# Optimization experiments

Measured on AMD Instinct MI355X. Metric: run time of the kernel, lower is better.

## Reference

```python
import jax, jax.numpy as jnp
import numpy as np

H = 8
HID = 512
DH = HID // H
EPS = 1e-5


def _ln(x, g, b):
    mu = jnp.mean(x, axis=-1, keepdims=True)
    var = jnp.mean(jnp.square(x - mu), axis=-1, keepdims=True)
    return (x - mu) * jax.lax.rsqrt(var + EPS) * g + b


def setup_inputs() -> dict:
    key = jax.random.key(0)
    ks = jax.random.split(key, 40)
    L, M, P, D = 4096, 1024, 4096, 512

    def xav(k, shp):
        lim = np.sqrt(6.0 / (shp[0] + shp[1]))
        return jax.random.uniform(k, shp, jnp.float32, -lim, lim)

    inp = {
        'lncRNA_embedding': jax.random.normal(ks[0], (L, D), jnp.float32),
        'miRNA_embedding': jax.random.normal(ks[1], (M, D), jnp.float32),
        'protein_embedding': jax.random.normal(ks[2], (P, D), jnp.float32),
        'lncRNA_miRNA_matrix': jax.random.randint(ks[3], (L, M), 0, 2, jnp.int32),
        'protein_miRNA_matrix': jax.random.randint(ks[4], (P, M), 0, 2, jnp.int32),
    }
    names = ['Wl', 'Wm', 'Wp', 'Wql', 'Wkl', 'Wvl', 'Wqp', 'Wkp', 'Wvp']
    for i, n in enumerate(names):
        inp[n] = xav(ks[5 + i], (HID, HID))
        inp['b' + n[1:]] = jnp.zeros((HID,), jnp.float32)
    inp['Wml'] = xav(ks[20], (2 * HID, D // 2))
    inp['bml'] = jnp.zeros((D // 2,), jnp.float32)
    inp['Wmp'] = xav(ks[21], (2 * HID, D // 2))
    inp['bmp'] = jnp.zeros((D // 2,), jnp.float32)
    inp['g1'] = jnp.ones((D // 2,), jnp.float32)
    inp['be1'] = jnp.zeros((D // 2,), jnp.float32)
    inp['g2'] = jnp.ones((D // 2,), jnp.float32)
    inp['be2'] = jnp.zeros((D // 2,), jnp.float32)
    # first three linears take dim-D input (D == HID here)
    return inp


def reference(lncRNA_embedding, miRNA_embedding, protein_embedding,
              lncRNA_miRNA_matrix, protein_miRNA_matrix,
              Wl, bl, Wm, bm, Wp, bp,
              Wql, bql, Wkl, bkl, Wvl, bvl,
              Wqp, bqp, Wkp, bkp, Wvp, bvp,
              Wml, bml, Wmp, bmp, g1, be1, g2, be2):
    L = lncRNA_embedding.shape[0]
    M = miRNA_embedding.shape[0]
    P = protein_embedding.shape[0]

    lt = lncRNA_embedding @ Wl + bl          # [L, HID]
    mt = miRNA_embedding @ Wm + bm           # [M, HID]
    pt = protein_embedding @ Wp + bp         # [P, HID]

    def heads(x, W, b, n):
        return (x @ W + b).reshape(n, H, DH)

    Ql = heads(lt, Wql, bql, L)              # [L, H, DH]
    Kl = heads(mt, Wkl, bkl, M)
    Vl = heads(mt, Wvl, bvl, M)
    Qp = heads(pt, Wqp, bqp, P)
    Kp = heads(mt, Wkp, bkp, M)
    Vp = heads(mt, Wvp, bvp, M)

    scale = 1.0 / np.sqrt(DH)
    sl = jnp.einsum('lhd,mhd->hlm', Ql, Kl) * scale      # [H, L, M]
    sl = jnp.where(lncRNA_miRNA_matrix[None] == 0, -1e9, sl)
    awl = jax.nn.softmax(sl, axis=-1)

    sp = jnp.einsum('phd,mhd->hpm', Qp, Kp) * scale      # [H, P, M]
    sp = jnp.where(protein_miRNA_matrix[None] == 0, -1e9, sp)
    awp = jax.nn.softmax(sp, axis=-1)

    ctx_l = jax.nn.relu(jnp.einsum('hlm,mhd->lhd', awl, Vl).reshape(L, HID))
    ctx_p = jax.nn.relu(jnp.einsum('hpm,mhd->phd', awp, Vp).reshape(P, HID))

    mutual = jnp.einsum('hlm,hpm->lp', awl, awp) / H     # [L, P]

    fin_l = ctx_l + mutual @ ctx_p
    fin_p = ctx_p + mutual.T @ ctx_l

    out_l = _ln(jnp.concatenate([lt, fin_l], axis=-1) @ Wml + bml, g1, be1)
    out_p = _ln(jnp.concatenate([fin_p, pt], axis=-1) @ Wmp + bmp, g2, be2)
    return out_l, out_p
```

## Files before the change

### kernel.cpp

```cpp
#include <hip/hip_runtime.h>
#include <hip/hip_bf16.h>

using bf16 = __hip_bfloat16;
typedef __attribute__((ext_vector_type(8))) short short8;
typedef __attribute__((ext_vector_type(4))) float floatx4;
typedef __attribute__((ext_vector_type(8))) unsigned short ushort8;
typedef __attribute__((ext_vector_type(4))) int i32x4;
typedef __attribute__((ext_vector_type(8))) int i32x8;

__device__ __forceinline__ float b2f(unsigned short u) {
    union { unsigned int i; float f; } x; x.i = ((unsigned int)u) << 16; return x.f;
}

__device__ __forceinline__ void async16(const void* g, void* l) {
    __builtin_amdgcn_global_load_lds((const __attribute__((address_space(1))) void*)g,
                                     (__attribute__((address_space(3))) void*)l,
                                     16, 0, 0);
}

__device__ __forceinline__ unsigned char f2e4m3(float f) {
    unsigned s = (__float_as_uint(f) >> 24) & 0x80u;
    f = fminf(fabsf(f), 448.f);
    if (f < 0.015625f) {
        int d = (int)rintf(f * 512.f);
        return (unsigned char)(s | (unsigned)d);
    }
    int E = (int)((__float_as_uint(f) >> 23) & 255u) - 127;
    float ulp_inv = __uint_as_float((unsigned)(127 + 3 - E) << 23);
    int m = (int)rintf(f * ulp_inv);
    int n = (m == 16) ? ((E + 8) << 3) : (((E + 7) << 3) + (m - 8));
    if (n > 0x7E) n = 0x7E;
    return (unsigned char)(s | (unsigned)n);
}

__device__ __forceinline__ bool sniff_wave(const unsigned short* p) {
    const int lane = threadIdx.x & 63;
    int wild = 0;
#pragma unroll
    for (int j = 0; j < 4; ++j) {
        float a = fabsf(b2f(p[lane * 4 + j]));
        wild += !(a <= 1e4f);
    }
#pragma unroll
    for (int o = 1; o < 64; o <<= 1) wild += __shfl_xor(wild, o);
    return wild > 16;
}

struct Cvt { const void* src; bf16* dst; int n; };
struct PrepArgs {
    Cvt cv[18];
    const void* tsrc[11];
    bf16* tdst[11];
    const unsigned short* sn;
};

__global__ __launch_bounds__(256) void prep(PrepArgs a) {
    const bool f32 = sniff_wave(a.sn);
    const int y = blockIdx.y;
    __shared__ bf16 tile[32][33];

    if (y < 18) {
        const Cvt c = a.cv[y];
        const int stride = gridDim.x * 256 * 8;
        for (int i = (blockIdx.x * 256 + threadIdx.x) * 8; i < c.n; i += stride) {
            if (f32) {
                const float* s = (const float*)c.src + i;
#pragma unroll
                for (int j = 0; j < 8; ++j) c.dst[i + j] = __float2bfloat16(s[j]);
            } else {
                *(ushort8*)((unsigned short*)c.dst + i) =
                    *(const ushort8*)((const unsigned short*)c.src + i);
            }
        }
        return;
    }

    const int tx = threadIdx.x & 31;
    const int ty = threadIdx.x >> 5;
    if (y < 27) {
        const void* in = a.tsrc[y - 18];
        bf16* out = a.tdst[y - 18];
        const int bc = (blockIdx.x & 15) * 32;
        const int br = (blockIdx.x >> 4) * 32;
#pragma unroll
        for (int i = 0; i < 32; i += 8) {
            const size_t idx = (size_t)(br + ty + i) * 512 + bc + tx;
            tile[ty + i][tx] = f32 ? __float2bfloat16(((const float*)in)[idx])
                                   : ((const bf16*)in)[idx];
        }
        __syncthreads();
#pragma unroll
        for (int i = 0; i < 32; i += 8)
            out[(size_t)(bc + ty + i) * 512 + br + tx] = tile[tx][ty + i];
    } else {
        const void* in = a.tsrc[y - 27 + 9];
        bf16* out = a.tdst[y - 27 + 9];
        const int bc = (blockIdx.x & 7) * 32;
        const int br = (blockIdx.x >> 3) * 32;
#pragma unroll
        for (int i = 0; i < 32; i += 8) {
            const size_t idx = (size_t)(br + ty + i) * 256 + bc + tx;
            tile[ty + i][tx] = f32 ? __float2bfloat16(((const float*)in)[idx])
                                   : ((const bf16*)in)[idx];
        }
        __syncthreads();
#pragma unroll
        for (int i = 0; i < 32; i += 8)
            out[(size_t)(bc + ty + i) * 1024 + br + tx] = tile[tx][ty + i];
    }
}

struct SegTab { const bf16* W[3]; const bf16* bias[3]; bf16* C[3]; int ldc[3]; int rs[3]; };

__global__ __launch_bounds__(256) void gemm_bt_seg(
    const bf16* __restrict__ A, SegTab T, int K)
{
    constexpr int TM = 2, TN = 2;
    __align__(16) __shared__ bf16 As[64 * 64];
    __align__(16) __shared__ bf16 Bs[64 * 64];

    const int lane = threadIdx.x & 63;
    const int wv   = threadIdx.x >> 6;
    const int gm   = blockIdx.y * 64;
    const int seg  = (gm >= 5120) ? 2 : ((gm >= 4096) ? 1 : 0);
    const bf16* B  = T.W[seg];
    const bf16* bias = T.bias[seg];
    bf16* C        = T.C[seg];
    const int ldc  = T.ldc[seg];
    const int m_base = gm - T.rs[seg];
    const int n_base = blockIdx.x * 64;
    const int wm0 = (wv >> 1) * 32;
    const int wn0 = (wv & 1) * 32;

    floatx4 zero = {0.f, 0.f, 0.f, 0.f};
    floatx4 acc[TM][TN];
#pragma unroll
    for (int mt = 0; mt < TM; ++mt)
#pragma unroll
        for (int nt = 0; nt < TN; ++nt) acc[mt][nt] = zero;

    const int sr  = lane >> 3;
    const int sce = ((lane & 7) ^ sr) * 8;
    const int fr  = lane & 15;
    const int q   = lane >> 4;
    const int sw  = fr & 7;

    for (int k0 = 0; k0 < K; k0 += 64) {
#pragma unroll
        for (int cc = 0; cc < 2; ++cc) {
            const int r0t = (wv + cc * 4) * 8;
            async16(A + (size_t)(gm + r0t + sr) * 512 + k0 + sce, &As[r0t * 64]);
            async16(B + (size_t)(n_base + r0t + sr) * 512 + k0 + sce, &Bs[r0t * 64]);
        }
        __syncthreads();
#pragma unroll
        for (int s = 0; s < 2; ++s) {
            const int off = ((s * 4 + q) ^ sw) * 8;
            short8 af[TM], bfr[TN];
#pragma unroll
            for (int mt = 0; mt < TM; ++mt)
                af[mt] = *(const short8*)&As[(wm0 + mt * 16 + fr) * 64 + off];
#pragma unroll
            for (int nt = 0; nt < TN; ++nt)
                bfr[nt] = *(const short8*)&Bs[(wn0 + nt * 16 + fr) * 64 + off];
#pragma unroll
            for (int mt = 0; mt < TM; ++mt)
#pragma unroll
                for (int nt = 0; nt < TN; ++nt)
                    acc[mt][nt] = __builtin_amdgcn_mfma_f32_16x16x32_bf16(
                        af[mt], bfr[nt], acc[mt][nt], 0, 0, 0);
        }
        __syncthreads();
    }

    const int er = lane >> 4;
    const int ec = lane & 15;
#pragma unroll
    for (int nt = 0; nt < TN; ++nt) {
        const int col = n_base + wn0 + nt * 16 + ec;
        const float bv = __bfloat162float(bias[col]);
#pragma unroll
        for (int mt = 0; mt < TM; ++mt)
#pragma unroll
            for (int r = 0; r < 4; ++r) {
                const int row = m_base + wm0 + mt * 16 + er * 4 + r;
                C[(size_t)row * ldc + col] = __float2bfloat16(acc[mt][nt][r] + bv);
            }
    }
}

struct BtArgs { const bf16* A; const bf16* B; void* C; const bf16* bias;
                int lda, ldb, ldc; };
struct BtSet { BtArgs s[3]; };

template <bool F32OUT, bool REMAP2>
__global__ __launch_bounds__(256) void gemm_btx(BtSet P, int K, float scale)
{
    constexpr int TM = 2, TN = 2;
    __align__(16) __shared__ bf16 As[64 * 64];
    __align__(16) __shared__ bf16 Bs[64 * 64];

    const BtArgs g = P.s[blockIdx.z];
    int bx = blockIdx.x, by = blockIdx.y;
    if (REMAP2 && blockIdx.z == 2) {
        const int flat = by * gridDim.x + bx;
        bx = flat & 31; by = flat >> 5;
    }
    const int lane = threadIdx.x & 63;
    const int wv   = threadIdx.x >> 6;
    const int m_base = by * 64;
    const int n_base = bx * 64;
    const int wm0 = (wv >> 1) * 32;
    const int wn0 = (wv & 1) * 32;

    floatx4 zero = {0.f, 0.f, 0.f, 0.f};
    floatx4 acc[TM][TN];
#pragma unroll
    for (int mt = 0; mt < TM; ++mt)
#pragma unroll
        for (int nt = 0; nt < TN; ++nt) acc[mt][nt] = zero;

    const int sr  = lane >> 3;
    const int sce = ((lane & 7) ^ sr) * 8;
    const int fr  = lane & 15;
    const int q   = lane >> 4;
    const int sw  = fr & 7;

    for (int k0 = 0; k0 < K; k0 += 64) {
#pragma unroll
        for (int cc = 0; cc < 2; ++cc) {
            const int r0t = (wv + cc * 4) * 8;
            async16(g.A + (size_t)(m_base + r0t + sr) * g.lda + k0 + sce, &As[r0t * 64]);
            async16(g.B + (size_t)(n_base + r0t + sr) * g.ldb + k0 + sce, &Bs[r0t * 64]);
        }
        __syncthreads();
#pragma unroll
        for (int s = 0; s < 2; ++s) {
            const int off = ((s * 4 + q) ^ sw) * 8;
            short8 af[TM], bfr[TN];
#pragma unroll
            for (int mt = 0; mt < TM; ++mt)
                af[mt] = *(const short8*)&As[(wm0 + mt * 16 + fr) * 64 + off];
#pragma unroll
            for (int nt = 0; nt < TN; ++nt)
                bfr[nt] = *(const short8*)&Bs[(wn0 + nt * 16 + fr) * 64 + off];
#pragma unroll
            for (int mt = 0; mt < TM; ++mt)
#pragma unroll
                for (int nt = 0; nt < TN; ++nt)
                    acc[mt][nt] = __builtin_amdgcn_mfma_f32_16x16x32_bf16(
                        af[mt], bfr[nt], acc[mt][nt], 0, 0, 0);
        }
        __syncthreads();
    }

    const int er = lane >> 4;
    const int ec = lane & 15;
#pragma unroll
    for (int nt = 0; nt < TN; ++nt) {
        const int col = n_base + wn0 + nt * 16 + ec;
        const float bv = __bfloat162float(g.bias[col]);
#pragma unroll
        for (int mt = 0; mt < TM; ++mt)
#pragma unroll
            for (int r = 0; r < 4; ++r) {
                const int row = m_base + wm0 + mt * 16 + er * 4 + r;
                const float v = acc[mt][nt][r] * scale + bv;
                if constexpr (F32OUT)
                    ((float*)g.C)[(size_t)row * g.ldc + col] = v;
                else
                    ((bf16*)g.C)[(size_t)row * g.ldc + col] = __float2bfloat16(v);
            }
    }
}

struct ScArgs { const bf16* Q; const bf16* K; const int* mask; unsigned char* aw; };
struct ScSet { ScArgs s[2]; const bf16* vsrc[2]; unsigned char* vdst[2]; };

__global__ __launch_bounds__(256) void scores_v8(ScSet P, int ldk, float scale)
{
    __shared__ float wred[16][4];
    __shared__ float wsum[16][4];
    __shared__ float tile[32][33];

    if (blockIdx.z == 2) {
        const int flat = blockIdx.y * 256 + blockIdx.x;
        if (flat >= 1024) return;
        const int side = flat >> 9;
        const int rem  = flat & 511;
        const bf16* in = P.vsrc[side];
        unsigned char* out = P.vdst[side];
        const int bc = (rem & 15) * 32;
        const int br = (rem >> 4) * 32;
        const int tx = threadIdx.x & 31;
        const int ty = threadIdx.x >> 5;
#pragma unroll
        for (int i = 0; i < 32; i += 8)
            tile[ty + i][tx] =
                __bfloat162float(in[(size_t)(br + ty + i) * 2048 + bc + tx]) * 4.0f;
        __syncthreads();
#pragma unroll
        for (int i = 0; i < 32; i += 8)
            out[(size_t)(bc + ty + i) * 1024 + br + tx] = f2e4m3(tile[tx][ty + i]);
        return;
    }

    const ScArgs g = P.s[blockIdx.z];
    const int t    = threadIdx.x;
    const int lane = t & 63;
    const int w    = t >> 6;
    const int h    = blockIdx.y;
    const int r0   = blockIdx.x * 16;
    const int fr   = lane & 15;
    const int fq   = lane >> 4;
    const int cbase = w * 256;

    const short* Qs = (const short*)g.Q + (size_t)(r0 + fr) * 512 + h * 64 + fq * 8;
    short8 a0 = *(const short8*)(Qs);
    short8 a1 = *(const short8*)(Qs + 32);

    floatx4 accs[16];
    const short* Kb = (const short*)g.K + h * 64 + fq * 8;
#pragma unroll
    for (int c = 0; c < 16; ++c) {
        const int krow = cbase + c * 16 + fr;
        short8 b0 = *(const short8*)(Kb + (size_t)krow * ldk);
        short8 b1 = *(const short8*)(Kb + (size_t)krow * ldk + 32);
        floatx4 acc = {0.f, 0.f, 0.f, 0.f};
        acc = __builtin_amdgcn_mfma_f32_16x16x32_bf16(a0, b0, acc, 0, 0, 0);
        acc = __builtin_amdgcn_mfma_f32_16x16x32_bf16(a1, b1, acc, 0, 0, 0);
        accs[c] = acc;
    }

    float mxr[4] = {-3e38f, -3e38f, -3e38f, -3e38f};
#pragma unroll
    for (int c = 0; c < 16; ++c) {
        const int col = cbase + c * 16 + fr;
#pragma unroll
        for (int r = 0; r < 4; ++r) {
            const int row = r0 + fq * 4 + r;
            float v = (g.mask[(size_t)row * 1024 + col] == 0) ? -1e9f
                                                              : accs[c][r] * scale;
            accs[c][r] = v;
            mxr[r] = fmaxf(mxr[r], v);
        }
    }
#pragma unroll
    for (int o = 1; o < 16; o <<= 1)
#pragma unroll
        for (int r = 0; r < 4; ++r) mxr[r] = fmaxf(mxr[r], __shfl_xor(mxr[r], o));
    if (fr == 0)
#pragma unroll
        for (int r = 0; r < 4; ++r) wred[fq * 4 + r][w] = mxr[r];
    __syncthreads();

    float mx[4], sm[4] = {0.f, 0.f, 0.f, 0.f};
#pragma unroll
    for (int r = 0; r < 4; ++r) {
        const int row = fq * 4 + r;
        mx[r] = fmaxf(fmaxf(wred[row][0], wred[row][1]),
                      fmaxf(wred[row][2], wred[row][3]));
    }
#pragma unroll
    for (int c = 0; c < 16; ++c)
#pragma unroll
        for (int r = 0; r < 4; ++r) {
            float e = __expf(accs[c][r] - mx[r]);
            accs[c][r] = e;
            sm[r] += e;
        }
#pragma unroll
    for (int o = 1; o < 16; o <<= 1)
#pragma unroll
        for (int r = 0; r < 4; ++r) sm[r] += __shfl_xor(sm[r], o);
    if (fr == 0)
#pragma unroll
        for (int r = 0; r < 4; ++r) wsum[fq * 4 + r][w] = sm[r];
    __syncthreads();

    float inv[4];
#pragma unroll
    for (int r = 0; r < 4; ++r) {
        const int row = fq * 4 + r;
        inv[r] = 32.0f / (wsum[row][0] + wsum[row][1] + wsum[row][2] + wsum[row][3]);
    }
#pragma unroll
    for (int c = 0; c < 16; ++c) {
        const int col = cbase + c * 16 + fr;
#pragma unroll
        for (int r = 0; r < 4; ++r) {
            const int row = r0 + fq * 4 + r;
            g.aw[(size_t)row * 8192 + h * 1024 + col] = f2e4m3(accs[c][r] * inv[r]);
        }
    }
}

struct B8Args { const unsigned char* A; const unsigned char* B; bf16* C;
                unsigned char* CT; };
struct B8Pair { B8Args s[2]; };

__global__ __launch_bounds__(256) void gemm_bt8_ctx(
    B8Pair P, int lda, long long a_kshift, int ldb, int ldc, int ldct,
    int K, float scale)
{
    constexpr int TM = 2, TN = 2;
    __align__(16) __shared__ unsigned char As[64 * 64];
    __align__(16) __shared__ unsigned char Bs[64 * 64];

    const B8Args g = P.s[blockIdx.z];
    const int lane = threadIdx.x & 63;
    const int wv   = threadIdx.x >> 6;
    const int m_base = blockIdx.y * 64;
    const int n_base = blockIdx.x * 64;
    const unsigned char* A = g.A + (long long)blockIdx.x * a_kshift;

    const int wm0 = (wv >> 1) * 32;
    const int wn0 = (wv & 1) * 32;

    floatx4 zero = {0.f, 0.f, 0.f, 0.f};
    floatx4 acc[TM][TN];
#pragma unroll
    for (int mt = 0; mt < TM; ++mt)
#pragma unroll
        for (int nt = 0; nt < TN; ++nt) acc[mt][nt] = zero;

    const int ar = lane >> 2;
    const int ac = (((lane & 3) ^ (ar & 3)) * 16);
    const int fr = lane & 15;
    const int q  = lane >> 4;
    const int sw = fr & 3;

    for (int k0 = 0; k0 < K; k0 += 64) {
        async16(A + (size_t)(m_base + wv * 16 + ar) * lda + k0 + ac, &As[wv * 16 * 64]);
        async16(g.B + (size_t)(n_base + wv * 16 + ar) * ldb + k0 + ac, &Bs[wv * 16 * 64]);
        __syncthreads();
#pragma unroll
        for (int s = 0; s < 2; ++s) {
            const int boff = (((s * 2 + (q >> 1)) ^ sw) * 16) + (q & 1) * 8;
            long af[TM], bfr[TN];
#pragma unroll
            for (int mt = 0; mt < TM; ++mt)
                af[mt] = *(const long*)&As[(wm0 + mt * 16 + fr) * 64 + boff];
#pragma unroll
            for (int nt = 0; nt < TN; ++nt)
                bfr[nt] = *(const long*)&Bs[(wn0 + nt * 16 + fr) * 64 + boff];
#pragma unroll
            for (int mt = 0; mt < TM; ++mt)
#pragma unroll
                for (int nt = 0; nt < TN; ++nt)
                    acc[mt][nt] = __builtin_amdgcn_mfma_f32_16x16x32_fp8_fp8(
                        af[mt], bfr[nt], acc[mt][nt], 0, 0, 0);
        }
        __syncthreads();
    }

    const int er = lane >> 4;
    const int ec = lane & 15;
#pragma unroll
    for (int nt = 0; nt < TN; ++nt) {
        const int col = n_base + wn0 + nt * 16 + ec;
#pragma unroll
        for (int mt = 0; mt < TM; ++mt) {
            const int rowb = m_base + wm0 + mt * 16 + er * 4;
            unsigned int pk = 0;
#pragma unroll
            for (int r = 0; r < 4; ++r) {
                float v = fmaxf(acc[mt][nt][r] * scale, 0.f);
                g.C[(size_t)(rowb + r) * ldc + col] = __float2bfloat16(v);
                pk |= (unsigned)f2e4m3(v * 16.0f) << (8 * r);
            }
            *(unsigned int*)(g.CT + (size_t)col * ldct + rowb) = pk;
        }
    }
}

__global__ __launch_bounds__(512, 2) void gemm_mutual(
    const unsigned char* __restrict__ A, const unsigned char* __restrict__ B,
    unsigned char* __restrict__ C, unsigned char* __restrict__ CT,
    int K, float scale)
{
    constexpr int BM = 256, BN = 256;
    constexpr int TM = 8, TN = 4;

    __align__(16) __shared__ unsigned char As[2][BM * 128];
    __align__(16) __shared__ unsigned char Bs[2][BN * 128];

    const int lane = threadIdx.x & 63;
    const int wv   = threadIdx.x >> 6;
    const int m_base = blockIdx.y * BM;
    const int n_base = blockIdx.x * BN;
    const int wm0 = (wv >> 2) * 128;
    const int wn0 = (wv & 3) * 64;

    floatx4 zero = {0.f, 0.f, 0.f, 0.f};
    floatx4 acc[TM][TN];
#pragma unroll
    for (int mt = 0; mt < TM; ++mt)
#pragma unroll
        for (int nt = 0; nt < TN; ++nt) acc[mt][nt] = zero;

    const int sr = lane >> 3;
    const int sc = ((lane & 7) ^ sr) * 16;
    const int fr = lane & 15;
    const int q  = lane >> 4;
    const int sw = fr & 7;

    const int NT = K >> 7;

    auto stage = [&](int t, int b) {
        const int k0 = t << 7;
#pragma unroll
        for (int cc = 0; cc < 4; ++cc) {
            const int r0t = (wv + cc * 8) * 8;
            async16(A + (size_t)(m_base + r0t + sr) * (size_t)K + k0 + sc,
                    &As[b][r0t * 128]);
            async16(B + (size_t)(n_base + r0t + sr) * (size_t)K + k0 + sc,
                    &Bs[b][r0t * 128]);
        }
    };

    stage(0, 0);
    stage(1, 1);

    for (int t = 0; t < NT; ++t) {
        const int cur = t & 1;
        if (t + 1 < NT)
            asm volatile("s_waitcnt vmcnt(8)\n\ts_barrier" ::: "memory");
        else
            asm volatile("s_waitcnt vmcnt(0)\n\ts_barrier" ::: "memory");

        i32x8 bfr[TN];
#pragma unroll
        for (int nt = 0; nt < TN; ++nt) {
            const unsigned char* rp = &Bs[cur][(wn0 + nt * 16 + fr) * 128];
            i32x4 lo = *(const i32x4*)(rp + (((q * 2 + 0) ^ sw) * 16));
            i32x4 hi = *(const i32x4*)(rp + (((q * 2 + 1) ^ sw) * 16));
            bfr[nt] = __builtin_shufflevector(lo, hi, 0, 1, 2, 3, 4, 5, 6, 7);
        }
        __builtin_amdgcn_s_setprio(1);
#pragma unroll
        for (int mt = 0; mt < TM; ++mt) {
            const unsigned char* rp = &As[cur][(wm0 + mt * 16 + fr) * 128];
            i32x4 lo = *(const i32x4*)(rp + (((q * 2 + 0) ^ sw) * 16));
            i32x4 hi = *(const i32x4*)(rp + (((q * 2 + 1) ^ sw) * 16));
            i32x8 af = __builtin_shufflevector(lo, hi, 0, 1, 2, 3, 4, 5, 6, 7);
#pragma unroll
            for (int nt = 0; nt < TN; ++nt)
                acc[mt][nt] = __builtin_amdgcn_mfma_scale_f32_16x16x128_f8f6f4(
                    af, bfr[nt], acc[mt][nt], 0, 0, 0, 127, 0, 127);
        }
        __builtin_amdgcn_s_setprio(0);
        asm volatile("s_barrier" ::: "memory");
        if (t + 2 < NT) stage(t + 2, cur);
    }

    const int er = lane >> 4;
    const int ec = lane & 15;
#pragma unroll
    for (int nt = 0; nt < TN; ++nt) {
        const int col = n_base + wn0 + nt * 16 + ec;
#pragma unroll
        for (int mt = 0; mt < TM; ++mt) {
            const int rowb = m_base + wm0 + mt * 16 + er * 4;
            unsigned int pk = 0;
#pragma unroll
            for (int r = 0; r < 4; ++r) {
                const unsigned char qv = f2e4m3(acc[mt][nt][r] * scale);
                C[(size_t)(rowb + r) * 4096 + col] = qv;
                pk |= (unsigned)qv << (8 * r);
            }
            *(unsigned int*)(CT + (size_t)col * 4096 + rowb) = pk;
        }
    }
}

struct MxArgs { const unsigned char* A; const unsigned char* B; void* C;
                const bf16* Cz; unsigned char* CT; };
struct MxPair { MxArgs s[2]; };

template <int BM, int BN, bool ADDC0, bool FP8OUT, bool TOUT>
__global__ __launch_bounds__(256, 2) void gemm_bt8mx(
    MxPair P, int lda, int ldb, int ldc, int ldc0, int ldct, int K, float scale)
{
    constexpr int WM = BM / 2;
    constexpr int WN = BN / 2;
    constexpr int TM = WM / 16;
    constexpr int TN = WN / 16;

    __align__(16) __shared__ unsigned char As[BM * 128];
    __align__(16) __shared__ unsigned char Bs[BN * 128];

    const MxArgs g = P.s[blockIdx.z];
    const int lane = threadIdx.x & 63;
    const int wv   = threadIdx.x >> 6;
    const int m_base = blockIdx.y * BM;
    const int n_base = blockIdx.x * BN;

    const int wm0 = (wv >> 1) * WM;
    const int wn0 = (wv & 1) * WN;

    floatx4 zero = {0.f, 0.f, 0.f, 0.f};
    floatx4 acc[TM][TN];
#pragma unroll
    for (int mt = 0; mt < TM; ++mt)
#pragma unroll
        for (int nt = 0; nt < TN; ++nt) acc[mt][nt] = zero;

    const int sr = lane >> 3;
    const int sc = ((lane & 7) ^ sr) * 16;
    const int fr = lane & 15;
    const int q  = lane >> 4;
    const int sw = fr & 7;

    for (int k0 = 0; k0 < K; k0 += 128) {
#pragma unroll
        for (int cc = 0; cc < BM / 32; ++cc) {
            const int r0t = (wv + cc * 4) * 8;
            async16(g.A + (size_t)(m_base + r0t + sr) * lda + k0 + sc, &As[r0t * 128]);
        }
#pragma unroll
        for (int cc = 0; cc < BN / 32; ++cc) {
            const int r0t = (wv + cc * 4) * 8;
            async16(g.B + (size_t)(n_base + r0t + sr) * ldb + k0 + sc, &Bs[r0t * 128]);
        }
        __syncthreads();

        i32x8 af[TM];
#pragma unroll
        for (int mt = 0; mt < TM; ++mt) {
            const unsigned char* rp = &As[(wm0 + mt * 16 + fr) * 128];
            i32x4 lo = *(const i32x4*)(rp + (((q * 2 + 0) ^ sw) * 16));
            i32x4 hi = *(const i32x4*)(rp + (((q * 2 + 1) ^ sw) * 16));
            af[mt] = __builtin_shufflevector(lo, hi, 0, 1, 2, 3, 4, 5, 6, 7);
        }
#pragma unroll
        for (int nt = 0; nt < TN; ++nt) {
            const unsigned char* rp = &Bs[(wn0 + nt * 16 + fr) * 128];
            i32x4 lo = *(const i32x4*)(rp + (((q * 2 + 0) ^ sw) * 16));
            i32x4 hi = *(const i32x4*)(rp + (((q * 2 + 1) ^ sw) * 16));
            i32x8 bf8 = __builtin_shufflevector(lo, hi, 0, 1, 2, 3, 4, 5, 6, 7);
#pragma unroll
            for (int mt = 0; mt < TM; ++mt)
                acc[mt][nt] = __builtin_amdgcn_mfma_scale_f32_16x16x128_f8f6f4(
                    af[mt], bf8, acc[mt][nt], 0, 0, 0, 127, 0, 127);
        }
        __syncthreads();
    }

    const int er = lane >> 4;
    const int ec = lane & 15;
#pragma unroll
    for (int nt = 0; nt < TN; ++nt) {
        const int col = n_base + wn0 + nt * 16 + ec;
#pragma unroll
        for (int mt = 0; mt < TM; ++mt) {
            const int rowb = m_base + wm0 + mt * 16 + er * 4;
            unsigned int pk = 0;
#pragma unroll
            for (int r = 0; r < 4; ++r) {
                float v = acc[mt][nt][r] * scale;
                if constexpr (ADDC0)
                    v += __bfloat162float(g.Cz[(size_t)(rowb + r) * ldc0 + col]);
                if constexpr (FP8OUT) {
                    const unsigned char qv = f2e4m3(v);
                    ((unsigned char*)g.C)[(size_t)(rowb + r) * ldc + col] = qv;
                    if constexpr (TOUT) pk |= (unsigned)qv << (8 * r);
                } else {
                    ((bf16*)g.C)[(size_t)(rowb + r) * ldc + col] = __float2bfloat16(v);
                }
            }
            if constexpr (TOUT)
                *(unsigned int*)(g.CT + (size_t)col * ldct + rowb) = pk;
        }
    }
}

__global__ __launch_bounds__(256) void ln_all(
    const float* __restrict__ X,
    const bf16* __restrict__ g1, const bf16* __restrict__ be1,
    const bf16* __restrict__ g2, const bf16* __restrict__ be2,
    void* __restrict__ out, const unsigned short* __restrict__ sn)
{
    const bool f32 = sniff_wave(sn);
    const int lane = threadIdx.x & 63;
    const int wv   = threadIdx.x >> 6;
    const int row  = blockIdx.x * 4 + wv;
    const bf16* gg = (row >= 4096) ? g2 : g1;
    const bf16* bb = (row >= 4096) ? be2 : be1;
    const float* x = X + (size_t)row * 256;
    float v[4], s = 0.f, s2 = 0.f;
#pragma unroll
    for (int i = 0; i < 4; ++i) {
        v[i] = x[lane + 64 * i];
        s += v[i]; s2 += v[i] * v[i];
    }
#pragma unroll
    for (int o = 1; o < 64; o <<= 1) { s += __shfl_xor(s, o); s2 += __shfl_xor(s2, o); }
    const float mu  = s * (1.0f / 256.0f);
    const float var = fmaxf(s2 * (1.0f / 256.0f) - mu * mu, 0.0f);
    const float inv = rsqrtf(var + 1e-5f);
#pragma unroll
    for (int i = 0; i < 4; ++i) {
        const int c = lane + 64 * i;
        const float y = (v[i] - mu) * inv * __bfloat162float(gg[c]) + __bfloat162float(bb[c]);
        if (f32) ((float*)out)[(size_t)row * 256 + c] = y;
        else     ((bf16*)out)[(size_t)row * 256 + c] = __float2bfloat16(y);
    }
}

extern "C" void kernel_launch(void* const* d_in, const int* in_sizes, int n_in,
                              void* d_out, int out_size, void* d_ws, size_t ws_size,
                              hipStream_t stream)
{
    const int L = 4096, Mm = 1024, P = 4096;

    const int* mask_l = (const int*)d_in[3];
    const int* mask_p = (const int*)d_in[4];
    const unsigned short* sn = (const unsigned short*)d_in[0];

    char* ws = (char*)d_ws;
    size_t off = 0;
    auto alloc = [&](size_t bytes) {
        void* p = ws + off; off += (bytes + 255) & ~(size_t)255; return p;
    };

    bf16* wt_all = (bf16*)alloc((size_t)9 * 512 * 512 * 2);
    bf16* WmlT   = (bf16*)alloc(1024 * 256 * 2);
    bf16* WmpT   = (bf16*)alloc(1024 * 256 * 2);
    bf16* b_l    = (bf16*)alloc(512 * 2);
    bf16* b_m    = (bf16*)alloc(512 * 2);
    bf16* b_p    = (bf16*)alloc(512 * 2);
    bf16* b_ql   = (bf16*)alloc(512 * 2);
    bf16* b_qp   = (bf16*)alloc(512 * 2);
    bf16* bcat   = (bf16*)alloc(2048 * 2);
    bf16* bml_c  = (bf16*)alloc(256 * 2);
    bf16* bmp_c  = (bf16*)alloc(256 * 2);
    bf16* g1c    = (bf16*)alloc(256 * 2);
    bf16* be1c   = (bf16*)alloc(256 * 2);
    bf16* g2c    = (bf16*)alloc(256 * 2);
    bf16* be2c   = (bf16*)alloc(256 * 2);
    bf16* emb_all = (bf16*)alloc((size_t)(L + Mm + P) * 512 * 2);
    bf16* embl   = emb_all;
    bf16* embm   = emb_all + (size_t)L * 512;
    bf16* embp   = embm + (size_t)Mm * 512;
    bf16* cat_l  = (bf16*)alloc((size_t)L * 1024 * 2);
    bf16* cat_p  = (bf16*)alloc((size_t)P * 1024 * 2);
    bf16* mt     = (bf16*)alloc((size_t)Mm * 512 * 2);
    bf16* Ql     = (bf16*)alloc((size_t)L * 512 * 2);
    bf16* Qp     = (bf16*)alloc((size_t)P * 512 * 2);
    bf16* kvcat  = (bf16*)alloc((size_t)Mm * 2048 * 2);
    unsigned char* V8lT = (unsigned char*)alloc((size_t)512 * Mm);
    unsigned char* V8pT = (unsigned char*)alloc((size_t)512 * Mm);
    bf16* ctx_l  = (bf16*)alloc((size_t)L * 512 * 2);
    bf16* ctx_p  = (bf16*)alloc((size_t)P * 512 * 2);
    unsigned char* ctx8lT = (unsigned char*)alloc((size_t)512 * L);
    unsigned char* ctx8pT = (unsigned char*)alloc((size_t)512 * P);
    unsigned char* mutual8  = (unsigned char*)alloc((size_t)L * P);
    unsigned char* mutual8T = (unsigned char*)alloc((size_t)L * P);
    unsigned char* awl8 = (unsigned char*)alloc((size_t)L * 8192);
    unsigned char* awp8 = (unsigned char*)alloc((size_t)P * 8192);
    float* tmp1 = (float*)awp8;

    PrepArgs pa;
    pa.sn = sn;
    pa.cv[0]  = { d_in[0],  embl, L * 512 };
    pa.cv[1]  = { d_in[1],  embm, Mm * 512 };
    pa.cv[2]  = { d_in[2],  embp, P * 512 };
    pa.cv[3]  = { d_in[6],  b_l,  512 };
    pa.cv[4]  = { d_in[8],  b_m,  512 };
    pa.cv[5]  = { d_in[10], b_p,  512 };
    pa.cv[6]  = { d_in[12], b_ql, 512 };
    pa.cv[7]  = { d_in[18], b_qp, 512 };
    pa.cv[8]  = { d_in[14], bcat,        512 };
    pa.cv[9]  = { d_in[16], bcat + 512,  512 };
    pa.cv[10] = { d_in[20], bcat + 1024, 512 };
    pa.cv[11] = { d_in[22], bcat + 1536, 512 };
    pa.cv[12] = { d_in[24], bml_c, 256 };
    pa.cv[13] = { d_in[26], bmp_c, 256 };
    pa.cv[14] = { d_in[27], g1c,  256 };
    pa.cv[15] = { d_in[28], be1c, 256 };
    pa.cv[16] = { d_in[29], g2c,  256 };
    pa.cv[17] = { d_in[30], be2c, 256 };
    const int slot_of[9] = {0, 1, 2, 3, 5, 6, 4, 7, 8};
    for (int i = 0; i < 9; ++i) {
        pa.tsrc[i] = d_in[5 + 2 * i];
        pa.tdst[i] = wt_all + (size_t)slot_of[i] * 512 * 512;
    }
    pa.tsrc[9]  = d_in[23]; pa.tdst[9]  = WmlT;
    pa.tsrc[10] = d_in[25]; pa.tdst[10] = WmpT;
    prep<<<dim3(256, 29), 256, 0, stream>>>(pa);

    bf16* WlT  = wt_all;
    bf16* WmT  = wt_all + (size_t)1 * 512 * 512;
    bf16* WpT  = wt_all + (size_t)2 * 512 * 512;
    bf16* WqlT = wt_all + (size_t)3 * 512 * 512;
    bf16* WqpT = wt_all + (size_t)4 * 512 * 512;
    bf16* WkvT = wt_all + (size_t)5 * 512 * 512;

    SegTab st;
    st.W[0] = WlT;  st.bias[0] = b_l; st.C[0] = cat_l;       st.ldc[0] = 1024; st.rs[0] = 0;
    st.W[1] = WmT;  st.bias[1] = b_m; st.C[1] = mt;          st.ldc[1] = 512;  st.rs[1] = 4096;
    st.W[2] = WpT;  st.bias[2] = b_p; st.C[2] = cat_p + 512; st.ldc[2] = 1024; st.rs[2] = 5120;
    gemm_bt_seg<<<dim3(8, 144), 256, 0, stream>>>(emb_all, st, 512);

    BtSet qs;
    qs.s[0] = { cat_l,       WqlT, Ql,    b_ql, 1024, 512, 512 };
    qs.s[1] = { cat_p + 512, WqpT, Qp,    b_qp, 1024, 512, 512 };
    qs.s[2] = { mt,          WkvT, kvcat, bcat, 512,  512, 2048 };
    gemm_btx<false, true><<<dim3(8, 64, 3), 256, 0, stream>>>(qs, 512, 1.0f);

    ScSet sc;
    sc.s[0] = { Ql, kvcat,        mask_l, awl8 };
    sc.s[1] = { Qp, kvcat + 1024, mask_p, awp8 };
    sc.vsrc[0] = kvcat + 512;  sc.vdst[0] = V8lT;
    sc.vsrc[1] = kvcat + 1536; sc.vdst[1] = V8pT;
    scores_v8<<<dim3(256, 8, 3), 256, 0, stream>>>(sc, 2048, 0.125f);

    B8Pair cx = { { { awl8, V8lT, ctx_l, ctx8lT },
                    { awp8, V8pT, ctx_p, ctx8pT } } };
    gemm_bt8_ctx<<<dim3(8, 64, 2), 256, 0, stream>>>(
        cx, 8192, 1024, 1024, 512, 4096, 1024, 1.0f / 128.0f);

    gemm_mutual<<<dim3(16, 16), 512, 0, stream>>>(
        awl8, awp8, mutual8, mutual8T, 8192, 0.03125f);

    MxPair fn = { { { mutual8,  ctx8pT, cat_l + 512, ctx_l, nullptr },
                    { mutual8T, ctx8lT, cat_p,       ctx_p, nullptr } } };
    gemm_bt8mx<64, 128, true, false, false><<<dim3(4, 64, 2), 256, 0, stream>>>(
        fn, 4096, 4096, 1024, 512, 0, 4096, 1.0f / 4096.0f);

    BtSet fp;
    fp.s[0] = { cat_l, WmlT, tmp1,                   bml_c, 1024, 1024, 256 };
    fp.s[1] = { cat_p, WmpT, tmp1 + (size_t)L * 256, bmp_c, 1024, 1024, 256 };
    fp.s[2] = fp.s[0];
    gemm_btx<true, false><<<dim3(4, 64, 2), 256, 0, stream>>>(fp, 1024, 1.0f);

    ln_all<<<dim3(2048), 256, 0, stream>>>(tmp1, g1c, be1c, g2c, be2c, d_out, sn);
}
```

Baseline: 521.2 us.

## Interleave mutual GEMM prefetch with MFMA phases and swizzle block order

The mutual FP8 GEMM main loop is restructured into four MFMA phases separated by barriers. The next K-tile's global-to-LDS loads are issued inside the first two phases, which replaces the two-tile-ahead prefetch with a one-ahead scheme that waits on vmcnt(0). Block indices are also remapped so that groups of eight consecutive blocks share A or B panels, which is meant to improve L2 reuse. The extra barriers and the shallower prefetch depth could expose load latency.

Result: no change. 525.4 us (+0.8%).

```diff
diff --git a/kernel.cpp b/kernel.cpp
--- a/kernel.cpp
+++ b/kernel.cpp
@@ -474,6 +474,20 @@
     }
 }
 
+#define MUT_PH_MFMA(M0, M1)                                                          \
+    __builtin_amdgcn_s_setprio(1);                                                   \
+    acc[M0][0] = __builtin_amdgcn_mfma_scale_f32_16x16x128_f8f6f4(aa0, bb0, acc[M0][0], 0, 0, 0, 127, 0, 127); \
+    acc[M0][1] = __builtin_amdgcn_mfma_scale_f32_16x16x128_f8f6f4(aa0, bb1, acc[M0][1], 0, 0, 0, 127, 0, 127); \
+    acc[M0][2] = __builtin_amdgcn_mfma_scale_f32_16x16x128_f8f6f4(aa0, bb2, acc[M0][2], 0, 0, 0, 127, 0, 127); \
+    acc[M0][3] = __builtin_amdgcn_mfma_scale_f32_16x16x128_f8f6f4(aa0, bb3, acc[M0][3], 0, 0, 0, 127, 0, 127); \
+    acc[M1][0] = __builtin_amdgcn_mfma_scale_f32_16x16x128_f8f6f4(aa1, bb0, acc[M1][0], 0, 0, 0, 127, 0, 127); \
+    acc[M1][1] = __builtin_amdgcn_mfma_scale_f32_16x16x128_f8f6f4(aa1, bb1, acc[M1][1], 0, 0, 0, 127, 0, 127); \
+    acc[M1][2] = __builtin_amdgcn_mfma_scale_f32_16x16x128_f8f6f4(aa1, bb2, acc[M1][2], 0, 0, 0, 127, 0, 127); \
+    acc[M1][3] = __builtin_amdgcn_mfma_scale_f32_16x16x128_f8f6f4(aa1, bb3, acc[M1][3], 0, 0, 0, 127, 0, 127); \
+    __builtin_amdgcn_s_setprio(0);
+
+#define MUT_BAR() asm volatile("s_barrier" ::: "memory")
+
 __global__ __launch_bounds__(512, 2) void gemm_mutual(
     const unsigned char* __restrict__ A, const unsigned char* __restrict__ B,
     unsigned char* __restrict__ C, unsigned char* __restrict__ CT,
@@ -487,8 +501,10 @@
 
     const int lane = threadIdx.x & 63;
     const int wv   = threadIdx.x >> 6;
-    const int m_base = blockIdx.y * BM;
-    const int n_base = blockIdx.x * BN;
+    const int bid0 = blockIdx.y * gridDim.x + blockIdx.x;
+    const int bswz = (bid0 & 7) * 32 + (bid0 >> 3);
+    const int m_base = (bswz >> 4) * BM;
+    const int n_base = (bswz & 15) * BN;
     const int wm0 = (wv >> 2) * 128;
     const int wn0 = (wv & 3) * 64;
 
@@ -507,51 +523,60 @@
 
     const int NT = K >> 7;
 
-    auto stage = [&](int t, int b) {
+    const unsigned char* Arow = A + (size_t)(m_base + sr) * (size_t)K + sc;
+    const unsigned char* Brow = B + (size_t)(n_base + sr) * (size_t)K + sc;
+
+    auto stage_pair = [&](int t, int b, int cc) {
         const int k0 = t << 7;
-#pragma unroll
-        for (int cc = 0; cc < 4; ++cc) {
-            const int r0t = (wv + cc * 8) * 8;
-            async16(A + (size_t)(m_base + r0t + sr) * (size_t)K + k0 + sc,
-                    &As[b][r0t * 128]);
-            async16(B + (size_t)(n_base + r0t + sr) * (size_t)K + k0 + sc,
-                    &Bs[b][r0t * 128]);
-        }
+        const int r0t = (wv + cc * 8) * 8;
+        async16(Arow + (size_t)r0t * K + k0, &As[b][r0t * 128]);
+        async16(Brow + (size_t)r0t * K + k0, &Bs[b][r0t * 128]);
     };
-
-    stage(0, 0);
-    stage(1, 1);
+    auto rdA = [&](int b, int mt) -> i32x8 {
+        const unsigned char* rp = &As[b][(wm0 + mt * 16 + fr) * 128];
+        i32x4 lo = *(const i32x4*)(rp + (((q * 2 + 0) ^ sw) * 16));
+        i32x4 hi = *(const i32x4*)(rp + (((q * 2 + 1) ^ sw) * 16));
+        return __builtin_shufflevector(lo, hi, 0, 1, 2, 3, 4, 5, 6, 7);
+    };
+    auto rdB = [&](int b, int nt) -> i32x8 {
+        const unsigned char* rp = &Bs[b][(wn0 + nt * 16 + fr) * 128];
+        i32x4 lo = *(const i32x4*)(rp + (((q * 2 + 0) ^ sw) * 16));
+        i32x4 hi = *(const i32x4*)(rp + (((q * 2 + 1) ^ sw) * 16));
+        return __builtin_shufflevector(lo, hi, 0, 1, 2, 3, 4, 5, 6, 7);
+    };
+
+#pragma unroll
+    for (int cc = 0; cc < 4; ++cc) stage_pair(0, 0, cc);
 
     for (int t = 0; t < NT; ++t) {
         const int cur = t & 1;
-        if (t + 1 < NT)
-            asm volatile("s_waitcnt vmcnt(8)\n\ts_barrier" ::: "memory");
-        else
-            asm volatile("s_waitcnt vmcnt(0)\n\ts_barrier" ::: "memory");
-
-        i32x8 bfr[TN];
-#pragma unroll
-        for (int nt = 0; nt < TN; ++nt) {
-            const unsigned char* rp = &Bs[cur][(wn0 + nt * 16 + fr) * 128];
-            i32x4 lo = *(const i32x4*)(rp + (((q * 2 + 0) ^ sw) * 16));
-            i32x4 hi = *(const i32x4*)(rp + (((q * 2 + 1) ^ sw) * 16));
-            bfr[nt] = __builtin_shufflevector(lo, hi, 0, 1, 2, 3, 4, 5, 6, 7);
-        }
-        __builtin_amdgcn_s_setprio(1);
-#pragma unroll
-        for (int mt = 0; mt < TM; ++mt) {
-            const unsigned char* rp = &As[cur][(wm0 + mt * 16 + fr) * 128];
-            i32x4 lo = *(const i32x4*)(rp + (((q * 2 + 0) ^ sw) * 16));
-            i32x4 hi = *(const i32x4*)(rp + (((q * 2 + 1) ^ sw) * 16));
-            i32x8 af = __builtin_shufflevector(lo, hi, 0, 1, 2, 3, 4, 5, 6, 7);
-#pragma unroll
-            for (int nt = 0; nt < TN; ++nt)
-                acc[mt][nt] = __builtin_amdgcn_mfma_scale_f32_16x16x128_f8f6f4(
-                    af, bfr[nt], acc[mt][nt], 0, 0, 0, 127, 0, 127);
-        }
-        __builtin_amdgcn_s_setprio(0);
-        asm volatile("s_barrier" ::: "memory");
-        if (t + 2 < NT) stage(t + 2, cur);
+        const int nxt = cur ^ 1;
+        const bool pf = (t + 1 < NT);
+        asm volatile("s_waitcnt vmcnt(0)" ::: "memory");
+        MUT_BAR();
+
+        i32x8 bb0 = rdB(cur, 0), bb1 = rdB(cur, 1);
+        i32x8 bb2 = rdB(cur, 2), bb3 = rdB(cur, 3);
+        i32x8 aa0 = rdA(cur, 0), aa1 = rdA(cur, 1);
+        if (pf) { stage_pair(t + 1, nxt, 0); stage_pair(t + 1, nxt, 1); }
+        MUT_BAR();
+        MUT_PH_MFMA(0, 1);
+        MUT_BAR();
+
+        aa0 = rdA(cur, 2); aa1 = rdA(cur, 3);
+        if (pf) { stage_pair(t + 1, nxt, 2); stage_pair(t + 1, nxt, 3); }
+        MUT_BAR();
+        MUT_PH_MFMA(2, 3);
+        MUT_BAR();
+
+        aa0 = rdA(cur, 4); aa1 = rdA(cur, 5);
+        MUT_BAR();
+        MUT_PH_MFMA(4, 5);
+        MUT_BAR();
+
+        aa0 = rdA(cur, 6); aa1 = rdA(cur, 7);
+        MUT_BAR();
+        MUT_PH_MFMA(6, 7);
     }
 
     const int er = lane >> 4;
```
